# Kernel optimization log

Hardware: AMD Instinct MI355X
Metric: run time of the kernel (lower is better)

The kernel has to match this reference:

```python
import jax, jax.numpy as jnp
import numpy as np

NUM_CLASSES = 10
LAMBDA_UNCERTAINTY = 0.5
IGNORE_INDEX = 10
B, H, W = 8, 512, 512


def setup_inputs() -> dict:
    key = jax.random.key(0)
    k1, k2 = jax.random.split(key)
    logits = jax.random.normal(k1, (B, NUM_CLASSES, H, W), dtype=jnp.float32)
    targets = jax.random.randint(k2, (B, H, W), 0, 11)  # includes ignore_index=10
    return {"logits": logits, "targets": targets}


def reference(logits, targets):
    C = NUM_CLASSES
    f32 = logits.dtype

    # entropy of the predicted distribution (torch adds 1e-8 inside log)
    probs = jax.nn.softmax(logits, axis=1)                      # [B,C,H,W]
    log_probs = jnp.log(probs + 1e-8)
    entropy = -jnp.sum(probs * log_probs, axis=1)               # [B,H,W]

    valid = targets != IGNORE_INDEX                             # [B,H,W] bool
    valid_f = valid.astype(f32)
    n_valid = jnp.sum(valid_f)                                  # scalar

    # single-pass scatter-mean replacing the per-class python loop
    t_clip = jnp.clip(targets, 0, C - 1)
    t_flat = t_clip.reshape(-1)
    v_flat = valid_f.reshape(-1)
    counts = jax.ops.segment_sum(v_flat, t_flat, num_segments=C)                    # n_c per class
    ent_sum = jax.ops.segment_sum(entropy.reshape(-1) * v_flat, t_flat, num_segments=C)

    has_samples = (counts > 0) & (n_valid > 0)
    w_base = jnp.where(has_samples, (n_valid - counts) / jnp.maximum(n_valid, 1.0), 0.0)
    entropy_mean = jnp.where(counts > 0, ent_sum / jnp.maximum(counts, 1.0), 0.0)
    w_combined = w_base * (1.0 + LAMBDA_UNCERTAINTY * entropy_mean)                 # [C]

    weight_map = w_combined[t_clip] * valid_f                   # [B,H,W]

    # per-pixel cross entropy, zeroed at ignore_index (torch F.cross_entropy semantics)
    log_sm = jax.nn.log_softmax(logits, axis=1)                 # [B,C,H,W]
    ce = -jnp.take_along_axis(log_sm, t_clip[:, None], axis=1)[:, 0]  # [B,H,W]
    ce = ce * valid_f

    return jnp.sum(ce * weight_map) / (n_valid + 1e-6)
```

## Files before the change

### kernel.cpp

```cpp
#include <hip/hip_runtime.h>

#define NCLS 10
#define IGN 10
#define HW_ (512 * 512)
#define BATCH 8
#define NPIX (BATCH * HW_)
#define THREADS 256
#define PIXPERTHREAD 4
#define CHUNKS 4
#define NBLOCKS (NPIX / (THREADS * PIXPERTHREAD * CHUNKS))
#define STAT_STRIDE 16
#define LAMBDA_UNC 0.5f

__global__ void awce_zero_stats(float* __restrict__ stats) {
    int i = threadIdx.x;
    if (i < 30 * STAT_STRIDE) stats[i] = 0.0f;
}

template <bool ATOMIC>
__global__ __launch_bounds__(THREADS) void awce_main(
    const float* __restrict__ logits,
    const int* __restrict__ targets,
    float* __restrict__ outbuf)
{
    const int tid = threadIdx.x;

    float cnt[NCLS], es[NCLS], cs[NCLS];
#pragma unroll
    for (int c = 0; c < NCLS; ++c) { cnt[c] = 0.f; es[c] = 0.f; cs[c] = 0.f; }

    float xb_[2][NCLS][4];
    int tb_[2][4];

    auto chunk_p0 = [&](int k) {
        return ((blockIdx.x * CHUNKS + k) * THREADS + tid) * PIXPERTHREAD;
    };

#define LOAD_CHUNK(k, slot)                                                        \
    {                                                                              \
        const int p0 = chunk_p0(k);                                                \
        const int b = p0 >> 18;                                                    \
        const int hw = p0 & (HW_ - 1);                                             \
        const float* base = logits + (size_t)b * (NCLS * (size_t)HW_) + hw;        \
        _Pragma("unroll")                                                          \
        for (int c = 0; c < NCLS; ++c) {                                           \
            float4 v = *reinterpret_cast<const float4*>(base + (size_t)c * HW_);   \
            xb_[slot][c][0] = v.x; xb_[slot][c][1] = v.y;                          \
            xb_[slot][c][2] = v.z; xb_[slot][c][3] = v.w;                          \
        }                                                                          \
        int4 t4 = *reinterpret_cast<const int4*>(targets + p0);                    \
        tb_[slot][0] = t4.x; tb_[slot][1] = t4.y;                                  \
        tb_[slot][2] = t4.z; tb_[slot][3] = t4.w;                                  \
    }

#define PROC_CHUNK(slot)                                                           \
    {                                                                              \
        _Pragma("unroll")                                                          \
        for (int j = 0; j < PIXPERTHREAD; ++j) {                                   \
            const int tj = tb_[slot][j];                                           \
            const bool valid = (tj != IGN);                                        \
            const int tc = valid ? tj : (NCLS - 1);                                \
            float m = xb_[slot][0][j];                                             \
            _Pragma("unroll")                                                      \
            for (int c = 1; c < NCLS; ++c) m = fmaxf(m, xb_[slot][c][j]);          \
            float s = 0.f, dot = 0.f, xt = 0.f;                                    \
            _Pragma("unroll")                                                      \
            for (int c = 0; c < NCLS; ++c) {                                       \
                const float xc = xb_[slot][c][j];                                  \
                const float e = __expf(xc - m);                                    \
                s += e;                                                            \
                dot = fmaf(e, xc, dot);                                            \
                xt = (tc == c) ? xc : xt;                                          \
            }                                                                      \
            const float lse = m + __logf(s);                                       \
            const float ent = lse - dot / s;                                       \
            const float ce = lse - xt;                                             \
            _Pragma("unroll")                                                      \
            for (int c = 0; c < NCLS; ++c) {                                       \
                const float match = (valid && (tc == c)) ? 1.f : 0.f;              \
                cnt[c] += match;                                                   \
                es[c] = fmaf(match, ent, es[c]);                                   \
                cs[c] = fmaf(match, ce, cs[c]);                                    \
            }                                                                      \
        }                                                                          \
    }

    LOAD_CHUNK(0, 0)
#pragma unroll
    for (int k = 0; k < CHUNKS; ++k) {
        if (k + 1 < CHUNKS) {
            if ((k + 1) & 1) LOAD_CHUNK(k + 1, 1) else LOAD_CHUNK(k + 1, 0)
        }
        if (k & 1) PROC_CHUNK(1) else PROC_CHUNK(0)
    }

#pragma unroll
    for (int c = 0; c < NCLS; ++c) {
#pragma unroll
        for (int o = 32; o >= 1; o >>= 1) {
            cnt[c] += __shfl_xor(cnt[c], o);
            es[c]  += __shfl_xor(es[c],  o);
            cs[c]  += __shfl_xor(cs[c],  o);
        }
    }

    __shared__ float red[THREADS / 64][30];
    const int wave = tid >> 6;
    const int lane = tid & 63;
    if (lane == 0) {
#pragma unroll
        for (int c = 0; c < NCLS; ++c) {
            red[wave][c]      = cnt[c];
            red[wave][10 + c] = es[c];
            red[wave][20 + c] = cs[c];
        }
    }
    __syncthreads();
    if (tid < 30) {
        float v = red[0][tid] + red[1][tid] + red[2][tid] + red[3][tid];
        if (ATOMIC) {
            atomicAdd(&outbuf[tid * STAT_STRIDE], v);
        } else {
            outbuf[tid * NBLOCKS + blockIdx.x] = v;
        }
    }
#undef LOAD_CHUNK
#undef PROC_CHUNK
}

__global__ __launch_bounds__(512) void awce_final_partials(
    const float* __restrict__ partials, float* __restrict__ out)
{
    __shared__ float sred[32];
    const int wave = threadIdx.x >> 6;
    const int lane = threadIdx.x & 63;
#pragma unroll
    for (int k = 0; k < 4; ++k) {
        const int c = wave + k * 8;
        if (c < 30) {
            const float* col = partials + (size_t)c * NBLOCKS;
            float s = 0.f;
#pragma unroll
            for (int i = 0; i < NBLOCKS / 64; ++i) s += col[lane + 64 * i];
#pragma unroll
            for (int o = 32; o >= 1; o >>= 1) s += __shfl_xor(s, o);
            if (lane == 0) sred[c] = s;
        }
    }
    __syncthreads();
    if (threadIdx.x == 0) {
        float cnt[NCLS], es[NCLS], cs[NCLS];
        float nv = 0.f;
#pragma unroll
        for (int c = 0; c < NCLS; ++c) {
            cnt[c] = sred[c];
            es[c]  = sred[10 + c];
            cs[c]  = sred[20 + c];
            nv += cnt[c];
        }
        float loss = 0.f;
#pragma unroll
        for (int c = 0; c < NCLS; ++c) {
            float wb = 0.f;
            if (cnt[c] > 0.f && nv > 0.f) wb = (nv - cnt[c]) / fmaxf(nv, 1.f);
            const float em = (cnt[c] > 0.f) ? es[c] / fmaxf(cnt[c], 1.f) : 0.f;
            const float wc = wb * (1.f + LAMBDA_UNC * em);
            loss = fmaf(cs[c], wc, loss);
        }
        out[0] = loss / (nv + 1e-6f);
    }
}

__global__ void awce_final_atomic(const float* __restrict__ stats, float* __restrict__ out) {
    if (threadIdx.x == 0) {
        float cnt[NCLS], es[NCLS], cs[NCLS];
        float nv = 0.f;
#pragma unroll
        for (int c = 0; c < NCLS; ++c) {
            cnt[c] = stats[c * STAT_STRIDE];
            es[c]  = stats[(10 + c) * STAT_STRIDE];
            cs[c]  = stats[(20 + c) * STAT_STRIDE];
            nv += cnt[c];
        }
        float loss = 0.f;
#pragma unroll
        for (int c = 0; c < NCLS; ++c) {
            float wb = 0.f;
            if (cnt[c] > 0.f && nv > 0.f) wb = (nv - cnt[c]) / fmaxf(nv, 1.f);
            const float em = (cnt[c] > 0.f) ? es[c] / fmaxf(cnt[c], 1.f) : 0.f;
            const float wc = wb * (1.f + LAMBDA_UNC * em);
            loss = fmaf(cs[c], wc, loss);
        }
        out[0] = loss / (nv + 1e-6f);
    }
}

extern "C" void kernel_launch(void* const* d_in, const int* in_sizes, int n_in,
                              void* d_out, int out_size, void* d_ws, size_t ws_size,
                              hipStream_t stream) {
    const float* logits = (const float*)d_in[0];
    const int* targets = (const int*)d_in[1];
    float* out = (float*)d_out;
    float* ws = (float*)d_ws;

    const size_t need = (size_t)30 * NBLOCKS * sizeof(float);
    if (ws_size >= need) {
        awce_main<false><<<NBLOCKS, THREADS, 0, stream>>>(logits, targets, ws);
        awce_final_partials<<<1, 512, 0, stream>>>(ws, out);
    } else {
        awce_zero_stats<<<1, 512, 0, stream>>>(ws);
        awce_main<true><<<NBLOCKS, THREADS, 0, stream>>>(logits, targets, ws);
        awce_final_atomic<<<1, 64, 0, stream>>>(ws, out);
    }
}
```

Baseline: 27.71 us.

## Replace per-class register accumulators with LDS privatized histograms

The kernel drops the 30 register accumulators per thread and their 30-way wave shuffle reduction. Per-pixel class counts, entropy and CE sums now go through LDS atomics into 32 privatized, padded histogram regions, and a short region sum finishes each block. It also moves exp/log/rcp to hardware exp2/log2/rcp intrinsics, halves chunks per block (doubling the block count), and sets a min-blocks launch bound to raise occupancy. LDS atomic contention and the per-block histogram zeroing and sync overhead could offset the register and shuffle savings.

After: 46.57 us. +68.0%, slower.

```diff
diff --git a/kernel.cpp b/kernel.cpp
--- a/kernel.cpp
+++ b/kernel.cpp
@@ -7,10 +7,16 @@
 #define NPIX (BATCH * HW_)
 #define THREADS 256
 #define PIXPERTHREAD 4
-#define CHUNKS 4
+#define CHUNKS 2
 #define NBLOCKS (NPIX / (THREADS * PIXPERTHREAD * CHUNKS))
 #define STAT_STRIDE 16
 #define LAMBDA_UNC 0.5f
+#define LOG2E 1.4426950408889634f
+#define LN2 0.6931471805599453f
+
+#define NREGION 32
+#define RSTRIDE 37
+#define HISTSZ (NREGION * RSTRIDE)
 
 __global__ void awce_zero_stats(float* __restrict__ stats) {
     int i = threadIdx.x;
@@ -18,16 +24,23 @@
 }
 
 template <bool ATOMIC>
-__global__ __launch_bounds__(THREADS) void awce_main(
+__global__ __launch_bounds__(THREADS, 4) void awce_main(
     const float* __restrict__ logits,
     const int* __restrict__ targets,
     float* __restrict__ outbuf)
 {
     const int tid = threadIdx.x;
 
-    float cnt[NCLS], es[NCLS], cs[NCLS];
-#pragma unroll
-    for (int c = 0; c < NCLS; ++c) { cnt[c] = 0.f; es[c] = 0.f; cs[c] = 0.f; }
+    __shared__ float hist[HISTSZ];
+#pragma unroll
+    for (int i = 0; i < (HISTSZ + THREADS - 1) / THREADS; ++i) {
+        const int idx = tid + i * THREADS;
+        if (idx < HISTSZ) hist[idx] = 0.0f;
+    }
+    __syncthreads();
+
+    const int region = ((tid >> 6) << 3) | ((tid >> 3) & 7);
+    float* hreg = &hist[region * RSTRIDE];
 
     float xb_[2][NCLS][4];
     int tb_[2][4];
@@ -63,69 +76,47 @@
             float m = xb_[slot][0][j];                                             \
             _Pragma("unroll")                                                      \
             for (int c = 1; c < NCLS; ++c) m = fmaxf(m, xb_[slot][c][j]);          \
+            const float nm2 = -m * LOG2E;                                          \
             float s = 0.f, dot = 0.f, xt = 0.f;                                    \
             _Pragma("unroll")                                                      \
             for (int c = 0; c < NCLS; ++c) {                                       \
                 const float xc = xb_[slot][c][j];                                  \
-                const float e = __expf(xc - m);                                    \
+                const float e = __builtin_amdgcn_exp2f(fmaf(xc, LOG2E, nm2));      \
                 s += e;                                                            \
                 dot = fmaf(e, xc, dot);                                            \
                 xt = (tc == c) ? xc : xt;                                          \
             }                                                                      \
-            const float lse = m + __logf(s);                                       \
-            const float ent = lse - dot / s;                                       \
+            const float lse = fmaf(__builtin_amdgcn_logf(s), LN2, m);              \
+            const float rs = __builtin_amdgcn_rcpf(s);                             \
+            const float ent = fmaf(-dot, rs, lse);                                 \
             const float ce = lse - xt;                                             \
-            _Pragma("unroll")                                                      \
-            for (int c = 0; c < NCLS; ++c) {                                       \
-                const float match = (valid && (tc == c)) ? 1.f : 0.f;              \
-                cnt[c] += match;                                                   \
-                es[c] = fmaf(match, ent, es[c]);                                   \
-                cs[c] = fmaf(match, ce, cs[c]);                                    \
+            if (valid) {                                                           \
+                atomicAdd(&hreg[tc], 1.0f);                                        \
+                atomicAdd(&hreg[10 + tc], ent);                                    \
+                atomicAdd(&hreg[20 + tc], ce);                                     \
             }                                                                      \
         }                                                                          \
     }
 
     LOAD_CHUNK(0, 0)
-#pragma unroll
-    for (int k = 0; k < CHUNKS; ++k) {
-        if (k + 1 < CHUNKS) {
-            if ((k + 1) & 1) LOAD_CHUNK(k + 1, 1) else LOAD_CHUNK(k + 1, 0)
-        }
-        if (k & 1) PROC_CHUNK(1) else PROC_CHUNK(0)
-    }
-
-#pragma unroll
-    for (int c = 0; c < NCLS; ++c) {
-#pragma unroll
-        for (int o = 32; o >= 1; o >>= 1) {
-            cnt[c] += __shfl_xor(cnt[c], o);
-            es[c]  += __shfl_xor(es[c],  o);
-            cs[c]  += __shfl_xor(cs[c],  o);
-        }
-    }
-
-    __shared__ float red[THREADS / 64][30];
-    const int wave = tid >> 6;
-    const int lane = tid & 63;
-    if (lane == 0) {
-#pragma unroll
-        for (int c = 0; c < NCLS; ++c) {
-            red[wave][c]      = cnt[c];
-            red[wave][10 + c] = es[c];
-            red[wave][20 + c] = cs[c];
-        }
-    }
+    LOAD_CHUNK(1, 1)
+    PROC_CHUNK(0)
+    PROC_CHUNK(1)
+#undef LOAD_CHUNK
+#undef PROC_CHUNK
+
     __syncthreads();
+
     if (tid < 30) {
-        float v = red[0][tid] + red[1][tid] + red[2][tid] + red[3][tid];
+        float v = 0.f;
+#pragma unroll
+        for (int r = 0; r < NREGION; ++r) v += hist[r * RSTRIDE + tid];
         if (ATOMIC) {
             atomicAdd(&outbuf[tid * STAT_STRIDE], v);
         } else {
             outbuf[tid * NBLOCKS + blockIdx.x] = v;
         }
     }
-#undef LOAD_CHUNK
-#undef PROC_CHUNK
 }
 
 __global__ __launch_bounds__(512) void awce_final_partials(
```
